# Optimization experiments

Hardware: AMD Instinct MI355X
Metric: run time of the kernel (lower is better)

The kernel has to match this reference:

```python
import jax, jax.numpy as jnp
import numpy as np

HEADS = 8
DIM_HEAD = 64


def setup_inputs() -> dict:
    key = jax.random.key(0)
    ks = jax.random.split(key, 5)
    B, N, C, coor = 2, 2048, 256, 3
    dim_inner = HEADS * DIM_HEAD  # 512
    # weight scale 1/16 ~ 1/sqrt(256) keeps softmax logits in a sane range
    w_scale = 1.0 / 16.0
    return {
        "x": jax.random.normal(ks[0], (B, N, C, coor), dtype=jnp.float32),
        "Wq": jax.random.normal(ks[1], (dim_inner, C), dtype=jnp.float32) * w_scale,
        "Wk": jax.random.normal(ks[2], (dim_inner, C), dtype=jnp.float32) * w_scale,
        "Wv": jax.random.normal(ks[3], (dim_inner, C), dtype=jnp.float32) * w_scale,
        "Wo": jax.random.normal(ks[4], (C, dim_inner), dtype=jnp.float32) * w_scale,
    }


def _split_heads(t, B, N, coor):
    # b n (h d) c -> b h n (d c)
    t = t.reshape(B, N, HEADS, DIM_HEAD, coor)
    t = t.transpose(0, 2, 1, 3, 4)
    return t.reshape(B, HEADS, N, DIM_HEAD * coor)


def reference(x, Wq, Wk, Wv, Wo):
    B, N, C, coor = x.shape
    # VNLinear: einsum('... i c, o i -> ... o c')
    q = jnp.einsum('bnic,oi->bnoc', x, Wq)
    k = jnp.einsum('bnic,oi->bnoc', x, Wk)
    v = jnp.einsum('bnic,oi->bnoc', x, Wv)
    q = _split_heads(q, B, N, coor)  # (B, H, N, d*c)
    k = _split_heads(k, B, N, coor)
    v = _split_heads(v, B, N, coor)
    scale = (DIM_HEAD * coor) ** -0.5
    sim = jnp.einsum('bhie,bhje->bhij', q, k) * scale  # (B, H, N, N)
    attn = jax.nn.softmax(sim, axis=-1)
    out = jnp.einsum('bhij,bhje->bhie', attn, v)  # (B, H, N, d*c)
    # b h n (d c) -> b n (h d) c
    out = out.reshape(B, HEADS, N, DIM_HEAD, coor).transpose(0, 2, 1, 3, 4)
    out = out.reshape(B, N, HEADS * DIM_HEAD, coor)
    # to_out VNLinear
    return jnp.einsum('bnic,oi->bnoc', out, Wo)  # (B, N, C, 3)
```

## Files before the change

### kernel.cpp

```cpp
#include <hip/hip_runtime.h>

#define HEADS 8
#define DH 64
#define CO 3
#define E 192
#define NSEQ 2048
#define BATCH 2
#define CIN 256
#define DINNER 512
#define NTOK 4096
#define BHTOT 16

typedef __attribute__((ext_vector_type(8))) short bf16x8;
typedef __attribute__((ext_vector_type(4))) short bf16x4;
typedef __attribute__((ext_vector_type(4))) float f32x4;
typedef __attribute__((ext_vector_type(4))) float float4v;

static __device__ inline short f2bf(float f) {
  union { float f; unsigned u; } v; v.f = f;
  unsigned r = (v.u + 0x7FFFu + ((v.u >> 16) & 1u)) >> 16;
  return (short)r;
}

static __device__ inline float bf2f(short s) {
  union { unsigned u; float f; } a;
  a.u = ((unsigned)(unsigned short)s) << 16;
  return a.f;
}

static __device__ inline void load_lds16(const short* g, short* l) {
  __builtin_amdgcn_global_load_lds(
      (const __attribute__((address_space(1))) void*)g,
      (__attribute__((address_space(3))) void*)l, 16, 0, 0);
}


__global__ __launch_bounds__(256) void prep(const float* __restrict__ x,
                                            const float* __restrict__ Wq,
                                            const float* __restrict__ Wk,
                                            const float* __restrict__ Wv,
                                            const float* __restrict__ Wo,
                                            short* __restrict__ xcp,
                                            short* __restrict__ wqkvp,
                                            short* __restrict__ wop) {
  int tid = threadIdx.x;
  if (blockIdx.x < 256) {
    __shared__ short st[12288];
    int mt = blockIdx.x;
    const float* xb = x + (size_t)mt * 12288;
#pragma unroll
    for (int r = 0; r < 12; r++) {
      int idx4 = r * 256 + tid;
      float4v v = *(const float4v*)(xb + idx4 * 4);
#pragma unroll
      for (int e = 0; e < 4; e++) {
        int fp = idx4 * 4 + e;
        int ti = fp / 3, c = fp - ti * 3;
        int tl = ti >> 8, i = ti & 255;
        int ks = i >> 5, qd = (i >> 3) & 3, j = i & 7;
        st[c * 4096 + ks * 512 + (qd * 16 + tl) * 8 + j] = f2bf(v[e]);
      }
    }
    __syncthreads();
    short* dst = xcp;
#pragma unroll
    for (int rep = 0; rep < 6; rep++) {
      int g = rep * 256 + tid;
      int c = g >> 9, rem = g & 511;
      *(bf16x8*)(dst + ((size_t)(c * 256 + mt) * 8) * 512 + rem * 8) =
          *(const bf16x8*)&st[c * 4096 + rem * 8];
    }
    return;
  }
  int idx = (blockIdx.x - 256) * 256 + tid;
  const float qscale = 0.07216878364870323f * 1.4426950408889634f;
  if (idx < 1536 * 256) {
    int o = idx >> 8, i = idx & 255;
    float v;
    if (o < 512) v = Wq[idx] * qscale;
    else if (o < 1024) v = Wk[idx - 512 * 256];
    else v = Wv[idx - 1024 * 256];
    int nt = o >> 4, ln = o & 15, ks = i >> 5, qd = (i >> 3) & 3, j = i & 7;
    wqkvp[((size_t)(nt * 8 + ks)) * 512 + (qd * 16 + ln) * 8 + j] = f2bf(v);
  } else {
    int j0 = idx - 1536 * 256;
    if (j0 < 256 * 512) {
      int o2 = j0 >> 9, i = j0 & 511;
      int nt = o2 >> 4, ln = o2 & 15, ks = i >> 5, qd = (i >> 3) & 3, j = i & 7;
      wop[((size_t)(nt * 16 + ks)) * 512 + (qd * 16 + ln) * 8 + j] = f2bf(Wo[j0]);
    }
  }
}

__global__ __launch_bounds__(256, 4) void qkv_gemm(const short* __restrict__ xcp,
                                                   const short* __restrict__ wqkvp,
                                                   short* __restrict__ qp,
                                                   short* __restrict__ kp,
                                                   short* __restrict__ vp) {
  __shared__ __align__(16) short pool[9216];
  int c = blockIdx.z, ntb = blockIdx.x, mtb = blockIdx.y;
  int tid = threadIdx.x, wave = tid >> 6, lane = tid & 63;
  int ln = lane & 15, quad = lane >> 4;
  int wm = wave >> 1, wn = wave & 1;

  const short* gA = xcp + ((size_t)(c * 256 + mtb * 8) * 8) * 512;

  f32x4 acc[4][2] = {};
#pragma unroll
  for (int i = 0; i < 2; i++) {
    int q = tid + 256 * i, mf = q >> 6, l = q & 63;
    load_lds16(gA + (size_t)(mf * 8) * 512 + l * 8, pool + q * 8);
  }
  for (int ks = 0; ks < 8; ks++) {
    int b = ks & 1;
    __syncthreads();
    if (ks < 7) {
#pragma unroll
      for (int i = 0; i < 2; i++) {
        int q = tid + 256 * i, mf = q >> 6, l = q & 63;
        load_lds16(gA + (size_t)(mf * 8 + ks + 1) * 512 + l * 8,
                   pool + (b ^ 1) * 4096 + q * 8);
      }
    }
    const short* As = pool + b * 4096;
    bf16x8 af[4], bfr[2];
#pragma unroll
    for (int j = 0; j < 2; j++)
      bfr[j] = *(const bf16x8*)(wqkvp +
          (size_t)((ntb * 4 + wn * 2 + j) * 8 + ks) * 512 + lane * 8);
#pragma unroll
    for (int i = 0; i < 4; i++) af[i] = *(const bf16x8*)&As[(wm * 4 + i) * 512 + lane * 8];
#pragma unroll
    for (int i = 0; i < 4; i++)
#pragma unroll
      for (int j = 0; j < 2; j++)
        acc[i][j] = __builtin_amdgcn_mfma_f32_16x16x32_bf16(af[i], bfr[j], acc[i][j], 0, 0, 0);
  }

  int mat = ntb >> 3;
  int h = ntb & 7;
  int b0 = mtb >> 4;
  int bhx = b0 * 8 + h;
  if (mat < 2) {
    __syncthreads();
    short* tp = pool;
#pragma unroll
    for (int i = 0; i < 4; i++)
#pragma unroll
      for (int j = 0; j < 2; j++)
#pragma unroll
        for (int jj = 0; jj < 4; jj++)
          tp[(wm * 64 + i * 16 + quad * 4 + jj) * 72 + wn * 32 + j * 16 + ln] =
              f2bf(acc[i][j][jj]);
    __syncthreads();
    short* dst = (mat == 0) ? qp : kp;
#pragma unroll
    for (int rep = 0; rep < 4; rep++) {
      int gi = rep * 256 + tid;
      int l2 = gi & 15, qd = (gi >> 4) & 3, nf2 = (gi >> 6) & 3,
          esp = (gi >> 8) & 1, kt2 = (gi >> 9) & 1;
      int tl = kt2 * 64 + nf2 * 16 + l2;
      bf16x8 val = *(const bf16x8*)&tp[tl * 72 + esp * 32 + qd * 8];
      int kt = (mtb * 2 + kt2) & 31;
      int es = c * 2 + esp;
      size_t off = (((size_t)((bhx * 32 + kt) * 24) + es * 4 + nf2) * 64 +
                    (size_t)(qd * 16 + l2)) * 8;
      *(bf16x8*)(dst + off) = val;
    }
  } else {
    int q2 = quad ^ (((quad ^ (quad >> 1)) & 1) * 3);
#pragma unroll
    for (int i = 0; i < 4; i++) {
      int kt = (mtb * 2 + wm) & 31;
      int ks2 = (i >> 1) & 1;
      int qd2 = (i * 2 + (q2 >> 1)) & 3;
#pragma unroll
      for (int j = 0; j < 2; j++) {
        int ef = c * 4 + wn * 2 + j;
        size_t off = ((size_t)((bhx * 32 + kt) * 24 + ks2 * 12 + ef)) * 512 +
                     (qd2 * 16 + ln) * 8 + (q2 & 1) * 4;
        bf16x4 val = { f2bf(acc[i][j][0]), f2bf(acc[i][j][1]),
                       f2bf(acc[i][j][2]), f2bf(acc[i][j][3]) };
        *(bf16x4*)(vp + off) = val;
      }
    }
  }
}

__global__ __launch_bounds__(256, 2) void attn(const short* __restrict__ qp,
                                               const short* __restrict__ kp,
                                               const short* __restrict__ vp,
                                               short* __restrict__ opart,
                                               float* __restrict__ lpart) {
  __shared__ __align__(16) short pool[25600];
  int pair = blockIdx.x, qt = blockIdx.y;
  int bh = pair & 15, kh = pair >> 4;
  int tid = threadIdx.x, wave = tid >> 6, lane = tid & 63;
  int ln = lane & 15, quad = lane >> 4;

  bf16x8 qf[2][6];
#pragma unroll
  for (int rg = 0; rg < 2; rg++) {
    int fi = wave * 2 + rg;
    const short* qb = qp +
        ((size_t)(bh * 32 + qt * 2 + (fi >> 2)) * 24 + (fi & 3)) * 512 + lane * 8;
#pragma unroll
    for (int es = 0; es < 6; es++) qf[rg][es] = *(const bf16x8*)(qb + es * 2048);
  }

  float l_r[2] = {0.f, 0.f};
  f32x4 acc[2][12] = {};
  bf16x8 pa[2] = {};
  const short* gKb = kp + (size_t)(bh * 32 + kh * 16) * 12288;
  const short* gVb = vp + (size_t)(bh * 32 + kh * 16) * 12288;

  auto stage_k = [&](int k32) {
    const short* g64 = gKb + (size_t)(k32 >> 1) * 12288;
    int half = k32 & 1;
    short* Kd = pool + (k32 & 1) * 6144;
#pragma unroll
    for (int i = 0; i < 3; i++) {
      int q = i * 256 + tid;
      int f = q >> 6, l = q & 63;
      int es = f >> 1, nfl = f & 1;
      load_lds16(g64 + (size_t)(es * 4 + half * 2 + nfl) * 512 + l * 8, Kd + q * 8);
    }
  };
  auto stage_v = [&](int k32) {
    const short* g64 = gVb + (size_t)(k32 >> 1) * 12288;
    int half = k32 & 1;
    short* Vd = pool + 12288 + (k32 & 1) * 6144;
#pragma unroll
    for (int i = 0; i < 3; i++) {
      int q = i * 256 + tid;
      int f = q >> 6, l = q & 63;
      load_lds16(g64 + (size_t)(half * 12 + f) * 512 + l * 8, Vd + q * 8);
    }
  };

  stage_k(0);
  for (int kt = 0; kt < 32; kt++) {
    int b = kt & 1;
    __syncthreads();
    if (kt < 31) stage_k(kt + 1);
    stage_v(kt);
    const short* Kl = pool + b * 6144;
    const short* Vl = pool + 12288 + ((kt - 1) & 1) * 6144;

    __builtin_amdgcn_s_setprio(1);
    f32x4 s[2][2] = {};
#pragma unroll
    for (int es = 0; es < 6; es++) {
#pragma unroll
      for (int nfl = 0; nfl < 2; nfl++) {
        bf16x8 kf = *(const bf16x8*)&Kl[(es * 2 + nfl) * 512 + lane * 8];
        s[0][nfl] = __builtin_amdgcn_mfma_f32_16x16x32_bf16(kf, qf[0][es], s[0][nfl], 0, 0, 0);
        s[1][nfl] = __builtin_amdgcn_mfma_f32_16x16x32_bf16(kf, qf[1][es], s[1][nfl], 0, 0, 0);
      }
    }
    if (kt > 0) {
#pragma unroll
      for (int ef = 0; ef < 12; ef++) {
        bf16x8 v0 = *(const bf16x8*)&Vl[ef * 512 + lane * 8];
        acc[0][ef] = __builtin_amdgcn_mfma_f32_16x16x32_bf16(pa[0], v0, acc[0][ef], 0, 0, 0);
        acc[1][ef] = __builtin_amdgcn_mfma_f32_16x16x32_bf16(pa[1], v0, acc[1][ef], 0, 0, 0);
      }
    }
    __builtin_amdgcn_s_setprio(0);

#pragma unroll
    for (int rg = 0; rg < 2; rg++) {
      float p0[4], p1[4];
#pragma unroll
      for (int jj = 0; jj < 4; jj++) {
        float e0 = __builtin_amdgcn_exp2f(s[rg][0][jj]);
        float e1 = __builtin_amdgcn_exp2f(s[rg][1][jj]);
        p0[jj] = e0; p1[jj] = e1;
        l_r[rg] += e0;
        l_r[rg] += e1;
      }
      unsigned a0, a1, b0, b1;
      asm("v_cvt_pk_bf16_f32 %0, %1, %2" : "=v"(a0) : "v"(p0[0]), "v"(p0[1]));
      asm("v_cvt_pk_bf16_f32 %0, %1, %2" : "=v"(a1) : "v"(p0[2]), "v"(p0[3]));
      asm("v_cvt_pk_bf16_f32 %0, %1, %2" : "=v"(b0) : "v"(p1[0]), "v"(p1[1]));
      asm("v_cvt_pk_bf16_f32 %0, %1, %2" : "=v"(b1) : "v"(p1[2]), "v"(p1[3]));
      auto r0 = __builtin_amdgcn_permlane32_swap(a0, b0, false, false);
      auto r1 = __builtin_amdgcn_permlane32_swap(a1, b1, false, false);
      union { unsigned u[4]; bf16x8 v; } pk;
      pk.u[0] = r0[0]; pk.u[1] = r1[0]; pk.u[2] = r0[1]; pk.u[3] = r1[1];
      pa[rg] = pk.v;
    }
  }

  __syncthreads();
  {
    const short* Vl = pool + 12288 + 6144;
#pragma unroll
    for (int ef = 0; ef < 12; ef++) {
      bf16x8 v0 = *(const bf16x8*)&Vl[ef * 512 + lane * 8];
      acc[0][ef] = __builtin_amdgcn_mfma_f32_16x16x32_bf16(pa[0], v0, acc[0][ef], 0, 0, 0);
      acc[1][ef] = __builtin_amdgcn_mfma_f32_16x16x32_bf16(pa[1], v0, acc[1][ef], 0, 0, 0);
    }
  }

#pragma unroll
  for (int rg = 0; rg < 2; rg++) {
    l_r[rg] += __shfl_xor(l_r[rg], 16, 64);
    l_r[rg] += __shfl_xor(l_r[rg], 32, 64);
  }

  __syncthreads();
  short* tp = pool;
#pragma unroll
  for (int rg = 0; rg < 2; rg++)
#pragma unroll
    for (int jj = 0; jj < 4; jj++) {
      int row = (wave * 2 + rg) * 16 + quad * 4 + jj;
#pragma unroll
      for (int ef = 0; ef < 12; ef++)
        tp[row * 200 + ef * 16 + ln] = f2bf(acc[rg][ef][jj]);
    }
  __syncthreads();
  const size_t obase = ((size_t)(kh * 16 + bh) * 2048 + qt * 128) * 192;
#pragma unroll
  for (int rep = 0; rep < 12; rep++) {
    int gi = rep * 256 + tid;
    int row = gi / 24, c8 = gi - row * 24;
    *(bf16x8*)(opart + obase + (size_t)row * 192 + c8 * 8) =
        *(const bf16x8*)&tp[row * 200 + c8 * 8];
  }
  int lb = (kh * 16 + bh) * 2048 + qt * 128;
  if (quad == 0) {
#pragma unroll
    for (int rg = 0; rg < 2; rg++)
      lpart[lb + (wave * 2 + rg) * 16 + ln] = l_r[rg];
  }
}

__global__ __launch_bounds__(256) void out_gemm(const short* __restrict__ opart,
                                                const float* __restrict__ lpart,
                                                const short* __restrict__ wop,
                                                float* __restrict__ out) {
  __shared__ __align__(16) float pool_f[12352];
  short* Al = (short*)pool_f;
  int mtb = blockIdx.x;
  int tid = threadIdx.x, wave = tid >> 6, lane = tid & 63;
  int ln = lane & 15, quad = lane >> 4;
  const size_t HSTR = (size_t)16 * 2048 * 192;

#pragma unroll
  for (int rep = 0; rep < 12; rep++) {
    int g = rep * 256 + tid;
    int c = g >> 10, inner = g & 1023;
    int d8 = inner & 7, h = (inner >> 3) & 7, row16 = inner >> 6;
    int t = mtb * 16 + row16, b = t >> 11, n = t & 2047;
    int bh = b * 8 + h;
    size_t src = ((size_t)bh * 2048 + n) * 192 + c * 64 + d8 * 8;
    bf16x8 o1 = *(const bf16x8*)(opart + src);
    bf16x8 o2 = *(const bf16x8*)(opart + HSTR + src);
    float l = lpart[bh * 2048 + n] + lpart[32768 + bh * 2048 + n];
    float inv = 1.f / l;
    bf16x8 r;
#pragma unroll
    for (int j = 0; j < 8; j++) r[j] = f2bf((bf2f(o1[j]) + bf2f(o2[j])) * inv);
    int ks = h * 2 + (d8 >> 2), qd = d8 & 3;
    *(bf16x8*)&Al[c * 8192 + ks * 512 + (qd * 16 + row16) * 8] = r;
  }
  __syncthreads();

  f32x4 acc[3][4] = {};
  for (int ks = 0; ks < 16; ks++) {
    bf16x8 af[3];
#pragma unroll
    for (int c = 0; c < 3; c++) af[c] = *(const bf16x8*)&Al[c * 8192 + ks * 512 + lane * 8];
#pragma unroll
    for (int jf = 0; jf < 4; jf++) {
      int nt = wave * 4 + jf;
      bf16x8 bfr = *(const bf16x8*)(wop + (size_t)(nt * 16 + ks) * 512 + lane * 8);
#pragma unroll
      for (int c = 0; c < 3; c++)
        acc[c][jf] = __builtin_amdgcn_mfma_f32_16x16x32_bf16(af[c], bfr, acc[c][jf], 0, 0, 0);
    }
  }
  __syncthreads();
#pragma unroll
  for (int c = 0; c < 3; c++)
#pragma unroll
    for (int jf = 0; jf < 4; jf++) {
      int o2 = (wave * 4 + jf) * 16 + ln;
#pragma unroll
      for (int jj = 0; jj < 4; jj++)
        pool_f[(quad * 4 + jj) * 772 + o2 * 3 + c] = acc[c][jf][jj];
    }
  __syncthreads();
  float* ob = out + (size_t)mtb * 12288;
#pragma unroll
  for (int rep = 0; rep < 12; rep++) {
    int idx = rep * 256 + tid;
    int row = idx / 192, col4 = idx - row * 192;
    *(float4v*)(ob + row * 768 + col4 * 4) =
        *(const float4v*)(pool_f + row * 772 + col4 * 4);
  }
}

extern "C" void kernel_launch(void* const* d_in, const int* in_sizes, int n_in,
                              void* d_out, int out_size, void* d_ws, size_t ws_size,
                              hipStream_t stream) {
  const float* x  = (const float*)d_in[0];
  const float* Wq = (const float*)d_in[1];
  const float* Wk = (const float*)d_in[2];
  const float* Wv = (const float*)d_in[3];
  const float* Wo = (const float*)d_in[4];
  float* out = (float*)d_out;

  short* ws    = (short*)d_ws;
  short* xcp   = ws;
  short* wqkvp = xcp + 3 * NTOK * CIN;
  short* wop   = wqkvp + 1536 * 256;
  short* qp    = wop + 256 * 512;
  short* kp    = qp + (size_t)BHTOT * NSEQ * E;
  short* vp    = kp + (size_t)BHTOT * NSEQ * E;
  short* opart = vp + (size_t)BHTOT * NSEQ * E;
  float* lpart = (float*)xcp;

  prep<<<2304, 256, 0, stream>>>(x, Wq, Wk, Wv, Wo, xcp, wqkvp, wop);
  qkv_gemm<<<dim3(24, 32, 3), 256, 0, stream>>>(xcp, wqkvp, qp, kp, vp);
  attn<<<dim3(32, 16), 256, 0, stream>>>(qp, kp, vp, opart, lpart);
  out_gemm<<<256, 256, 0, stream>>>(opart, lpart, wop, out);
}
```

Measured before the change: 154.8 us.

## Split attention keys four ways, shrink LDS for higher occupancy

Templates the attention kernel on the number of key splits and launches four splits when the workspace is large enough, doubling the block count. The V buffer becomes single-buffered, with an extra barrier per iteration, so LDS drops from 25600 to 18432 shorts and launch bounds allow four blocks per CU. The output transpose staging is done in two halves to fit the smaller pool. out_gemm sums an arbitrary number of partial outputs and normalizers, which costs more partial-output traffic and extra sync in exchange for more parallelism and occupancy.

```diff
diff --git a/kernel.cpp b/kernel.cpp
--- a/kernel.cpp
+++ b/kernel.cpp
@@ -187,12 +187,14 @@
   }
 }
 
-__global__ __launch_bounds__(256, 2) void attn(const short* __restrict__ qp,
+template<int NKH>
+__global__ __launch_bounds__(256, 4) void attn(const short* __restrict__ qp,
                                                const short* __restrict__ kp,
                                                const short* __restrict__ vp,
                                                short* __restrict__ opart,
                                                float* __restrict__ lpart) {
-  __shared__ __align__(16) short pool[25600];
+  constexpr int KITERS = 64 / NKH;
+  __shared__ __align__(16) short pool[18432];
   int pair = blockIdx.x, qt = blockIdx.y;
   int bh = pair & 15, kh = pair >> 4;
   int tid = threadIdx.x, wave = tid >> 6, lane = tid & 63;
@@ -211,8 +213,8 @@
   float l_r[2] = {0.f, 0.f};
   f32x4 acc[2][12] = {};
   bf16x8 pa[2] = {};
-  const short* gKb = kp + (size_t)(bh * 32 + kh * 16) * 12288;
-  const short* gVb = vp + (size_t)(bh * 32 + kh * 16) * 12288;
+  const short* gKb = kp + (size_t)(bh * 32 + kh * (32 / NKH)) * 12288;
+  const short* gVb = vp + (size_t)(bh * 32 + kh * (32 / NKH)) * 12288;
 
   auto stage_k = [&](int k32) {
     const short* g64 = gKb + (size_t)(k32 >> 1) * 12288;
@@ -229,7 +231,7 @@
   auto stage_v = [&](int k32) {
     const short* g64 = gVb + (size_t)(k32 >> 1) * 12288;
     int half = k32 & 1;
-    short* Vd = pool + 12288 + (k32 & 1) * 6144;
+    short* Vd = pool + 12288;
 #pragma unroll
     for (int i = 0; i < 3; i++) {
       int q = i * 256 + tid;
@@ -239,13 +241,11 @@
   };
 
   stage_k(0);
-  for (int kt = 0; kt < 32; kt++) {
-    int b = kt & 1;
-    __syncthreads();
-    if (kt < 31) stage_k(kt + 1);
-    stage_v(kt);
-    const short* Kl = pool + b * 6144;
-    const short* Vl = pool + 12288 + ((kt - 1) & 1) * 6144;
+  for (int kt = 0; kt < KITERS; kt++) {
+    __syncthreads();
+    if (kt < KITERS - 1) stage_k(kt + 1);
+    const short* Kl = pool + (kt & 1) * 6144;
+    const short* Vl = pool + 12288;
 
     __builtin_amdgcn_s_setprio(1);
     f32x4 s[2][2] = {};
@@ -267,6 +267,9 @@
       }
     }
     __builtin_amdgcn_s_setprio(0);
+
+    __syncthreads();
+    stage_v(kt);
 
 #pragma unroll
     for (int rg = 0; rg < 2; rg++) {
@@ -294,7 +297,7 @@
 
   __syncthreads();
   {
-    const short* Vl = pool + 12288 + 6144;
+    const short* Vl = pool + 12288;
 #pragma unroll
     for (int ef = 0; ef < 12; ef++) {
       bf16x8 v0 = *(const bf16x8*)&Vl[ef * 512 + lane * 8];
@@ -309,25 +312,27 @@
     l_r[rg] += __shfl_xor(l_r[rg], 32, 64);
   }
 
-  __syncthreads();
-  short* tp = pool;
-#pragma unroll
-  for (int rg = 0; rg < 2; rg++)
+  const size_t obase = ((size_t)(kh * 16 + bh) * 2048 + qt * 128) * 192;
+#pragma unroll
+  for (int rg = 0; rg < 2; rg++) {
+    __syncthreads();
+    short* tp = pool;
 #pragma unroll
     for (int jj = 0; jj < 4; jj++) {
-      int row = (wave * 2 + rg) * 16 + quad * 4 + jj;
+      int r4 = wave * 16 + quad * 4 + jj;
 #pragma unroll
       for (int ef = 0; ef < 12; ef++)
-        tp[row * 200 + ef * 16 + ln] = f2bf(acc[rg][ef][jj]);
-    }
-  __syncthreads();
-  const size_t obase = ((size_t)(kh * 16 + bh) * 2048 + qt * 128) * 192;
-#pragma unroll
-  for (int rep = 0; rep < 12; rep++) {
-    int gi = rep * 256 + tid;
-    int row = gi / 24, c8 = gi - row * 24;
-    *(bf16x8*)(opart + obase + (size_t)row * 192 + c8 * 8) =
-        *(const bf16x8*)&tp[row * 200 + c8 * 8];
+        tp[r4 * 200 + ef * 16 + ln] = f2bf(acc[rg][ef][jj]);
+    }
+    __syncthreads();
+#pragma unroll
+    for (int rep = 0; rep < 6; rep++) {
+      int gi = rep * 256 + tid;
+      int rowc = gi / 24, c8 = gi - rowc * 24;
+      int row = (rowc >> 4) * 32 + rg * 16 + (rowc & 15);
+      *(bf16x8*)(opart + obase + (size_t)row * 192 + c8 * 8) =
+          *(const bf16x8*)&tp[rowc * 200 + c8 * 8];
+    }
   }
   int lb = (kh * 16 + bh) * 2048 + qt * 128;
   if (quad == 0) {
@@ -337,6 +342,7 @@
   }
 }
 
+template<int NPART>
 __global__ __launch_bounds__(256) void out_gemm(const short* __restrict__ opart,
                                                 const float* __restrict__ lpart,
                                                 const short* __restrict__ wop,
@@ -356,13 +362,20 @@
     int t = mtb * 16 + row16, b = t >> 11, n = t & 2047;
     int bh = b * 8 + h;
     size_t src = ((size_t)bh * 2048 + n) * 192 + c * 64 + d8 * 8;
-    bf16x8 o1 = *(const bf16x8*)(opart + src);
-    bf16x8 o2 = *(const bf16x8*)(opart + HSTR + src);
-    float l = lpart[bh * 2048 + n] + lpart[32768 + bh * 2048 + n];
+    float l = 0.f;
+#pragma unroll
+    for (int p = 0; p < NPART; p++) l += lpart[((size_t)(p * 16 + bh)) * 2048 + n];
     float inv = 1.f / l;
+    float a8[8] = {};
+#pragma unroll
+    for (int p = 0; p < NPART; p++) {
+      bf16x8 o = *(const bf16x8*)(opart + (size_t)p * HSTR + src);
+#pragma unroll
+      for (int j = 0; j < 8; j++) a8[j] += bf2f(o[j]);
+    }
     bf16x8 r;
 #pragma unroll
-    for (int j = 0; j < 8; j++) r[j] = f2bf((bf2f(o1[j]) + bf2f(o2[j])) * inv);
+    for (int j = 0; j < 8; j++) r[j] = f2bf(a8[j] * inv);
     int ks = h * 2 + (d8 >> 2), qd = d8 & 3;
     *(bf16x8*)&Al[c * 8192 + ks * 512 + (qd * 16 + row16) * 8] = r;
   }
@@ -423,8 +436,18 @@
   short* opart = vp + (size_t)BHTOT * NSEQ * E;
   float* lpart = (float*)xcp;
 
+  const size_t base_shorts = (size_t)(3 * NTOK * CIN) + 1536 * 256 + 256 * 512 +
+                             3 * (size_t)BHTOT * NSEQ * E;
+  const size_t need4 = (base_shorts + 4 * (size_t)BHTOT * NSEQ * E) * sizeof(short);
+  bool p4 = ws_size >= need4;
+
   prep<<<2304, 256, 0, stream>>>(x, Wq, Wk, Wv, Wo, xcp, wqkvp, wop);
   qkv_gemm<<<dim3(24, 32, 3), 256, 0, stream>>>(xcp, wqkvp, qp, kp, vp);
-  attn<<<dim3(32, 16), 256, 0, stream>>>(qp, kp, vp, opart, lpart);
-  out_gemm<<<256, 256, 0, stream>>>(opart, lpart, wop, out);
-}
+  if (p4) {
+    attn<4><<<dim3(64, 16), 256, 0, stream>>>(qp, kp, vp, opart, lpart);
+    out_gemm<4><<<256, 256, 0, stream>>>(opart, lpart, wop, out);
+  } else {
+    attn<2><<<dim3(32, 16), 256, 0, stream>>>(qp, kp, vp, opart, lpart);
+    out_gemm<2><<<256, 256, 0, stream>>>(opart, lpart, wop, out);
+  }
+}
```

New measurement: 311.0 us. 2.01x slower.
